# Kernel tuning notes

Hardware: AMD Instinct MI355X
Metric: run time of the kernel (lower is better)

Reference implementation:

```python
import jax, jax.numpy as jnp
import numpy as np


def setup_inputs() -> dict:
    key = jax.random.key(0)
    k1, k2, k3, k4, k5 = jax.random.split(key, 5)
    B, S, K, N, G = 4, 2048, 4096, 4096, 64  # G = group_size -> num_groups = K // G = 64
    x = jax.random.normal(k1, (B, S, K), dtype=jnp.float32)
    # int2 codes stored one-per-int8 slot (low 2 bits valid); use int32 container
    weight_q = jax.random.randint(k2, (N, K), 0, 4, dtype=jnp.int32)
    scale = jax.random.uniform(k3, (N, K // G), dtype=jnp.float32) * 0.05 + 0.01
    zp = jax.random.uniform(k4, (N, K // G), dtype=jnp.float32) * 3.0
    bias = jax.random.normal(k5, (N,), dtype=jnp.float32)
    return {"x": x, "weight_q": weight_q, "scale": scale, "zp": zp, "bias": bias}


def _dequant(weight_q, scale, zp):
    # weight_q: [N, K] int codes in [0,4); scale/zp: [N, num_groups]
    N, K = weight_q.shape
    num_groups = scale.shape[1]
    gs = K // num_groups  # group_size
    q = weight_q.astype(jnp.float32).reshape(N, num_groups, gs)
    w = (q - zp[:, :, None]) * scale[:, :, None]
    return w.reshape(N, K)


def reference(x, weight_q, scale, zp, bias):
    # asymm_qw2_gemm: out = x @ dequant(W)^T + bias
    w = _dequant(weight_q, scale, zp)            # [N, K]
    out = jnp.einsum('bsk,nk->bsn', x, w)        # [B, S, N]
    return out + bias
```

## Files before the change

kernel.cpp:

```cpp
#include <hip/hip_runtime.h>
#include <stdint.h>


typedef __attribute__((ext_vector_type(4))) float  f32x4;
typedef __attribute__((ext_vector_type(4))) int    i32x4;
typedef __attribute__((ext_vector_type(8))) __bf16 bf16x8;
typedef __attribute__((ext_vector_type(4))) unsigned short u16x4;

__device__ __forceinline__ unsigned short f2bf(float f) {
  unsigned u = __builtin_bit_cast(unsigned, f);
  u += 0x7fffu + ((u >> 16) & 1u);
  return (unsigned short)(u >> 16);
}

__device__ __forceinline__ void async16(const void* g, void* l) {
  __builtin_amdgcn_global_load_lds(
      (const __attribute__((address_space(1))) unsigned int*)g,
      (__attribute__((address_space(3))) unsigned int*)l, 16, 0, 0);
}

__global__ __launch_bounds__(256) void prep_kernel(
    const float* __restrict__ x, unsigned short* __restrict__ xb, int xchunks,
    const int* __restrict__ wq, const float* __restrict__ scale,
    const float* __restrict__ zp, unsigned short* __restrict__ wb,
    int wchunks, int K, int G) {
  int xblocks = (xchunks + 255) >> 8;
  if ((int)blockIdx.x < xblocks) {
    int i = blockIdx.x * 256 + threadIdx.x;
    if (i >= xchunks) return;
    f32x4 a = ((const f32x4*)x)[i];
    u16x4 o;
    o[0] = f2bf(a[0]); o[1] = f2bf(a[1]); o[2] = f2bf(a[2]); o[3] = f2bf(a[3]);
    *(u16x4*)(xb + (size_t)i * 4) = o;
  } else {
    int i = (blockIdx.x - xblocks) * 256 + threadIdx.x;
    if (i >= wchunks) return;
    int k4 = i * 4;
    int n = k4 / K, kk = k4 % K;
    int ng = K / G;
    int g = kk / G;
    float s = scale[(size_t)n * ng + g];
    float b = -zp[(size_t)n * ng + g] * s;
    i32x4 qv = ((const i32x4*)wq)[i];
    u16x4 o;
    o[0] = f2bf((float)qv[0] * s + b); o[1] = f2bf((float)qv[1] * s + b);
    o[2] = f2bf((float)qv[2] * s + b); o[3] = f2bf((float)qv[3] * s + b);
    *(u16x4*)(wb + (size_t)i * 4) = o;
  }
}

#define BM 256
#define BN 256
#define BK 32
#define NBUF 4

__global__ __launch_bounds__(512, 2) void gemm_bt_kernel(
    const unsigned short* __restrict__ A,
    const unsigned short* __restrict__ B,
    const float* __restrict__ bias,
    float* __restrict__ C, int M, int N, int K) {
  __shared__ unsigned short As[NBUF * BM * BK];
  __shared__ unsigned short Bs[NBUF * BM * BK];

  const int tid  = threadIdx.x;
  const int lane = tid & 63;
  const int wave = tid >> 6;
  const int wm = wave >> 2, wn = wave & 3;
  const int q = lane >> 4, r = lane & 15;

  int id = blockIdx.x;
  {
    int nwg = gridDim.x;
    if ((nwg & 7) == 0) id = (id & 7) * (nwg >> 3) + (id >> 3);
  }
  const int nbx = N / BN;
  const int m0 = (id / nbx) * BM;
  const int n0 = (id % nbx) * BN;

  const int srow = tid >> 2;
  const int gch  = (tid & 3) ^ ((tid >> 3) & 3);
  const unsigned short* aG = A + (size_t)(m0 + srow) * K + gch * 8;
  const unsigned short* bG = B + (size_t)(n0 + srow) * K + gch * 8;
  const size_t rowblk = (size_t)128 * K;

  const int s0   = (q ^ ((r >> 1) & 3)) * 8;
  const int aOff = (wm * 128 + r) * BK + s0;
  const int bOff = (wn * 64  + r) * BK + s0;

  f32x4 acc[8][4] = {};
  const int NT = K / BK;

#define STAGE(bi, kk) { \
    unsigned short* al = As + (bi) * (BM * BK) + tid * 8; \
    unsigned short* bl = Bs + (bi) * (BM * BK) + tid * 8; \
    async16(aG + (kk), al);  async16(aG + rowblk + (kk), al + 4096); \
    async16(bG + (kk), bl);  async16(bG + rowblk + (kk), bl + 4096); }

  STAGE(0, 0)
  if (NT > 1) STAGE(1, BK)
  if (NT > 2) STAGE(2, 2 * BK)

#pragma unroll 1
  for (int t = 0; t < NT; ++t) {
    if (t + 3 < NT) STAGE((t + 3) & 3, (t + 3) * BK)
    if (t + 3 < NT)      asm volatile("s_waitcnt vmcnt(12)" ::: "memory");
    else if (t + 2 < NT) asm volatile("s_waitcnt vmcnt(8)"  ::: "memory");
    else if (t + 1 < NT) asm volatile("s_waitcnt vmcnt(4)"  ::: "memory");
    else                 asm volatile("s_waitcnt vmcnt(0)"  ::: "memory");
    __builtin_amdgcn_s_barrier();
    asm volatile("" ::: "memory");

    const int base = (t & 3) * (BM * BK);
    bf16x8 bfr[4], af0[4], af1[4];
#pragma unroll
    for (int j = 0; j < 4; ++j)
      bfr[j] = *(const bf16x8*)&Bs[base + bOff + j * 16 * BK];
#pragma unroll
    for (int i = 0; i < 4; ++i)
      af0[i] = *(const bf16x8*)&As[base + aOff + i * 16 * BK];

    __builtin_amdgcn_s_setprio(1);
#pragma unroll
    for (int i = 0; i < 4; ++i)
#pragma unroll
      for (int j = 0; j < 4; ++j)
        acc[i][j] = __builtin_amdgcn_mfma_f32_16x16x32_bf16(
            af0[i], bfr[j], acc[i][j], 0, 0, 0);
    __builtin_amdgcn_s_setprio(0);

#pragma unroll
    for (int i = 0; i < 4; ++i)
      af1[i] = *(const bf16x8*)&As[base + aOff + (4 + i) * 16 * BK];

    __builtin_amdgcn_s_setprio(1);
#pragma unroll
    for (int i = 0; i < 4; ++i)
#pragma unroll
      for (int j = 0; j < 4; ++j)
        acc[4 + i][j] = __builtin_amdgcn_mfma_f32_16x16x32_bf16(
            af1[i], bfr[j], acc[4 + i][j], 0, 0, 0);
    __builtin_amdgcn_s_setprio(0);

    asm volatile("" ::: "memory");
    __builtin_amdgcn_s_barrier();
  }

  float bv[4];
#pragma unroll
  for (int j = 0; j < 4; ++j) bv[j] = bias[n0 + wn * 64 + j * 16 + r];
#pragma unroll
  for (int i = 0; i < 8; ++i) {
    int mbase = m0 + wm * 128 + i * 16 + q * 4;
#pragma unroll
    for (int e = 0; e < 4; ++e) {
      float* crow = C + (size_t)(mbase + e) * N + n0 + wn * 64 + r;
#pragma unroll
      for (int j = 0; j < 4; ++j)
        crow[j * 16] = acc[i][j][e] + bv[j];
    }
  }
}

__global__ __launch_bounds__(256) void naive_kernel(
    const float* __restrict__ x, const int* __restrict__ wq,
    const float* __restrict__ scale, const float* __restrict__ zp,
    const float* __restrict__ bias, float* __restrict__ out,
    int M, int N, int K, int G) {
  int idx = blockIdx.x * 256 + threadIdx.x;
  if (idx >= M * N) return;
  int m = idx / N, n = idx % N;
  const float* xr = x + (size_t)m * K;
  const int* wr = wq + (size_t)n * K;
  int ng = K / G;
  float acc = 0.f;
  for (int g = 0; g < ng; ++g) {
    float s = scale[(size_t)n * ng + g];
    float b = -zp[(size_t)n * ng + g] * s;
    for (int k = 0; k < G; ++k)
      acc += xr[g * G + k] * ((float)wr[g * G + k] * s + b);
  }
  out[idx] = acc + bias[n];
}

extern "C" void kernel_launch(void* const* d_in, const int* in_sizes, int n_in,
                              void* d_out, int out_size, void* d_ws, size_t ws_size,
                              hipStream_t stream) {
  const float* x     = (const float*)d_in[0];
  const int*   wq    = (const int*)d_in[1];
  const float* scale = (const float*)d_in[2];
  const float* zp    = (const float*)d_in[3];
  const float* bias  = (const float*)d_in[4];
  float* out = (float*)d_out;

  const int N  = in_sizes[4];
  const int K  = in_sizes[1] / N;
  const int ng = in_sizes[2] / N;
  const int G  = K / ng;
  const int M  = in_sizes[0] / K;

  size_t xb_bytes = (size_t)M * K * 2;
  size_t wb_bytes = (size_t)N * K * 2;
  bool divisible = (M % BM == 0) && (N % BN == 0) && (K % BK == 0);
  if (ws_size < xb_bytes + wb_bytes || !divisible) {
    int total = M * N;
    naive_kernel<<<dim3((total + 255) / 256), dim3(256), 0, stream>>>(
        x, wq, scale, zp, bias, out, M, N, K, G);
    return;
  }

  unsigned short* xb = (unsigned short*)d_ws;
  unsigned short* wb = (unsigned short*)((char*)d_ws + xb_bytes);

  int xchunks = M * K / 4;
  int wchunks = N * K / 4;
  int xblocks = (xchunks + 255) / 256;
  int wblocks = (wchunks + 255) / 256;
  prep_kernel<<<dim3(xblocks + wblocks), dim3(256), 0, stream>>>(
      x, xb, xchunks, wq, scale, zp, wb, wchunks, K, G);

  dim3 grid((M / BM) * (N / BN));
  gemm_bt_kernel<<<grid, dim3(512), 0, stream>>>(xb, wb, bias, out, M, N, K);
}
```

Baseline: 622.0 us.

## Restructure GEMM main loop into ping-pong K=64 tiles with interleaved prefetch

Replaces the 4-deep ring of BK=32 stages with two ping-pong halves of a K=64 tile, each split into two 32-wide subregions. Global-to-LDS prefetches of the next tile are spread between the MFMA blocks, and one barrier per half-tile replaces the pair of barriers per stage. The aim is to halve loop iterations and cut barrier/waitcnt overhead while keeping loads overlapped with compute. The trade-off is a shallower prefetch distance (one tile ahead) and tighter hazard reasoning around the vmcnt counts and LDS buffer reuse.

After: 549.0 us. 1.13x faster.

```diff
diff --git a/kernel.cpp b/kernel.cpp
--- a/kernel.cpp
+++ b/kernel.cpp
@@ -51,16 +51,16 @@
 
 #define BM 256
 #define BN 256
-#define BK 32
-#define NBUF 4
+#define TK 64
+#define REG 8192
 
 __global__ __launch_bounds__(512, 2) void gemm_bt_kernel(
     const unsigned short* __restrict__ A,
     const unsigned short* __restrict__ B,
     const float* __restrict__ bias,
     float* __restrict__ C, int M, int N, int K) {
-  __shared__ unsigned short As[NBUF * BM * BK];
-  __shared__ unsigned short Bs[NBUF * BM * BK];
+  __shared__ unsigned short As[4 * REG];
+  __shared__ unsigned short Bs[4 * REG];
 
   const int tid  = threadIdx.x;
   const int lane = tid & 63;
@@ -81,68 +81,99 @@
   const int gch  = (tid & 3) ^ ((tid >> 3) & 3);
   const unsigned short* aG = A + (size_t)(m0 + srow) * K + gch * 8;
   const unsigned short* bG = B + (size_t)(n0 + srow) * K + gch * 8;
-  const size_t rowblk = (size_t)128 * K;
-
-  const int s0   = (q ^ ((r >> 1) & 3)) * 8;
-  const int aOff = (wm * 128 + r) * BK + s0;
-  const int bOff = (wn * 64  + r) * BK + s0;
+  const size_t rb = (size_t)128 * K;
+
+  unsigned short* aS = As + tid * 8;
+  unsigned short* bS = Bs + tid * 8;
+
+  const int qc8 = (q ^ ((r >> 1) & 3)) * 8;
+  const unsigned short* aRd = As + (wm * 128 + r) * 32 + qc8;
+  const unsigned short* bRd = Bs + (wn * 64  + r) * 32 + qc8;
 
   f32x4 acc[8][4] = {};
-  const int NT = K / BK;
-
-#define STAGE(bi, kk) { \
-    unsigned short* al = As + (bi) * (BM * BK) + tid * 8; \
-    unsigned short* bl = Bs + (bi) * (BM * BK) + tid * 8; \
-    async16(aG + (kk), al);  async16(aG + rowblk + (kk), al + 4096); \
-    async16(bG + (kk), bl);  async16(bG + rowblk + (kk), bl + 4096); }
-
-  STAGE(0, 0)
-  if (NT > 1) STAGE(1, BK)
-  if (NT > 2) STAGE(2, 2 * BK)
+  const int NT = K / TK;
+
+#define STG(S, G, par, kh, kk) { \
+    unsigned short* l = (S) + ((par) * 2 + (kh)) * REG; \
+    async16((G) + (kk) + (kh) * 32, l); \
+    async16((G) + rb + (kk) + (kh) * 32, l + 4096); }
+
+  STG(aS, aG, 0, 0, 0) STG(bS, bG, 0, 0, 0)
+  STG(aS, aG, 0, 1, 0) STG(bS, bG, 0, 1, 0)
 
 #pragma unroll 1
   for (int t = 0; t < NT; ++t) {
-    if (t + 3 < NT) STAGE((t + 3) & 3, (t + 3) * BK)
-    if (t + 3 < NT)      asm volatile("s_waitcnt vmcnt(12)" ::: "memory");
-    else if (t + 2 < NT) asm volatile("s_waitcnt vmcnt(8)"  ::: "memory");
-    else if (t + 1 < NT) asm volatile("s_waitcnt vmcnt(4)"  ::: "memory");
-    else                 asm volatile("s_waitcnt vmcnt(0)"  ::: "memory");
+    const int par = t & 1, nxt = par ^ 1;
+    const int kk1 = (t + 1) * TK;
+    const bool pf = (t + 1 < NT);
+
+    if (pf) STG(aS, aG, nxt, 0, kk1)
+    if (pf) asm volatile("s_waitcnt vmcnt(6)" ::: "memory");
+    else    asm volatile("s_waitcnt vmcnt(4)" ::: "memory");
     __builtin_amdgcn_s_barrier();
     asm volatile("" ::: "memory");
-
-    const int base = (t & 3) * (BM * BK);
-    bf16x8 bfr[4], af0[4], af1[4];
-#pragma unroll
-    for (int j = 0; j < 4; ++j)
-      bfr[j] = *(const bf16x8*)&Bs[base + bOff + j * 16 * BK];
-#pragma unroll
-    for (int i = 0; i < 4; ++i)
-      af0[i] = *(const bf16x8*)&As[base + aOff + i * 16 * BK];
-
-    __builtin_amdgcn_s_setprio(1);
-#pragma unroll
-    for (int i = 0; i < 4; ++i)
-#pragma unroll
-      for (int j = 0; j < 4; ++j)
-        acc[i][j] = __builtin_amdgcn_mfma_f32_16x16x32_bf16(
-            af0[i], bfr[j], acc[i][j], 0, 0, 0);
-    __builtin_amdgcn_s_setprio(0);
-
-#pragma unroll
-    for (int i = 0; i < 4; ++i)
-      af1[i] = *(const bf16x8*)&As[base + aOff + (4 + i) * 16 * BK];
-
-    __builtin_amdgcn_s_setprio(1);
-#pragma unroll
-    for (int i = 0; i < 4; ++i)
-#pragma unroll
-      for (int j = 0; j < 4; ++j)
-        acc[4 + i][j] = __builtin_amdgcn_mfma_f32_16x16x32_bf16(
-            af1[i], bfr[j], acc[4 + i][j], 0, 0, 0);
-    __builtin_amdgcn_s_setprio(0);
-
+    {
+      const unsigned short* a0 = aRd + par * 2 * REG;
+      const unsigned short* b0 = bRd + par * 2 * REG;
+      bf16x8 bf[4], af[4];
+#pragma unroll
+      for (int j = 0; j < 4; ++j) bf[j] = *(const bf16x8*)&b0[j * 512];
+#pragma unroll
+      for (int i = 0; i < 4; ++i) af[i] = *(const bf16x8*)&a0[i * 512];
+      __builtin_amdgcn_s_setprio(1);
+#pragma unroll
+      for (int i = 0; i < 4; ++i)
+#pragma unroll
+        for (int j = 0; j < 4; ++j)
+          acc[i][j] = __builtin_amdgcn_mfma_f32_16x16x32_bf16(
+              af[i], bf[j], acc[i][j], 0, 0, 0);
+      __builtin_amdgcn_s_setprio(0);
+      if (pf) STG(bS, bG, nxt, 0, kk1)
+#pragma unroll
+      for (int i = 0; i < 4; ++i) af[i] = *(const bf16x8*)&a0[(4 + i) * 512];
+      __builtin_amdgcn_s_setprio(1);
+#pragma unroll
+      for (int i = 0; i < 4; ++i)
+#pragma unroll
+        for (int j = 0; j < 4; ++j)
+          acc[4 + i][j] = __builtin_amdgcn_mfma_f32_16x16x32_bf16(
+              af[i], bf[j], acc[4 + i][j], 0, 0, 0);
+      __builtin_amdgcn_s_setprio(0);
+    }
+
+    if (pf) STG(aS, aG, nxt, 1, kk1)
+    if (pf) asm volatile("s_waitcnt vmcnt(6)" ::: "memory");
+    else    asm volatile("s_waitcnt vmcnt(0)" ::: "memory");
+    __builtin_amdgcn_s_barrier();
     asm volatile("" ::: "memory");
-    __builtin_amdgcn_s_barrier();
+    {
+      const unsigned short* a1 = aRd + (par * 2 + 1) * REG;
+      const unsigned short* b1 = bRd + (par * 2 + 1) * REG;
+      bf16x8 bf[4], af[4];
+#pragma unroll
+      for (int j = 0; j < 4; ++j) bf[j] = *(const bf16x8*)&b1[j * 512];
+#pragma unroll
+      for (int i = 0; i < 4; ++i) af[i] = *(const bf16x8*)&a1[i * 512];
+      __builtin_amdgcn_s_setprio(1);
+#pragma unroll
+      for (int i = 0; i < 4; ++i)
+#pragma unroll
+        for (int j = 0; j < 4; ++j)
+          acc[i][j] = __builtin_amdgcn_mfma_f32_16x16x32_bf16(
+              af[i], bf[j], acc[i][j], 0, 0, 0);
+      __builtin_amdgcn_s_setprio(0);
+      if (pf) STG(bS, bG, nxt, 1, kk1)
+#pragma unroll
+      for (int i = 0; i < 4; ++i) af[i] = *(const bf16x8*)&a1[(4 + i) * 512];
+      __builtin_amdgcn_s_setprio(1);
+#pragma unroll
+      for (int i = 0; i < 4; ++i)
+#pragma unroll
+        for (int j = 0; j < 4; ++j)
+          acc[4 + i][j] = __builtin_amdgcn_mfma_f32_16x16x32_bf16(
+              af[i], bf[j], acc[4 + i][j], 0, 0, 0);
+      __builtin_amdgcn_s_setprio(0);
+    }
   }
 
   float bv[4];
@@ -200,7 +231,7 @@
 
   size_t xb_bytes = (size_t)M * K * 2;
   size_t wb_bytes = (size_t)N * K * 2;
-  bool divisible = (M % BM == 0) && (N % BN == 0) && (K % BK == 0);
+  bool divisible = (M % BM == 0) && (N % BN == 0) && (K % TK == 0);
   if (ws_size < xb_bytes + wb_bytes || !divisible) {
     int total = M * N;
     naive_kernel<<<dim3((total + 255) / 256), dim3(256), 0, stream>>>(
```
